# Performance work log

Hardware: AMD Instinct MI355X
Metric: run time of the kernel (lower is better)

## Reference

```python
import math
import jax, jax.numpy as jnp
import numpy as np

N = 4096        # nodes
D = 256         # input_dim
H = 8           # n_heads
HD = D // H     # head_dim
E = 131072      # edges (avg degree 32)
LEAKY_ALPHA = 0.2  # tf.nn.leaky_relu default


def setup_inputs() -> dict:
    key = jax.random.key(0)
    ks = jax.random.split(key, 8)
    inputs = jax.random.normal(ks[0], (N, D), dtype=jnp.float32)
    src = jax.random.randint(ks[1], (E,), 0, N, dtype=jnp.int64)
    dst = jax.random.randint(ks[2], (E,), 0, N, dtype=jnp.int64)
    s = 1.0 / np.sqrt(D).astype(np.float32)
    WQ = jax.random.normal(ks[3], (D, D), dtype=jnp.float32) * s
    WK = jax.random.normal(ks[4], (D, D), dtype=jnp.float32) * s
    WV = jax.random.normal(ks[5], (D, D), dtype=jnp.float32) * s
    Wc = jax.random.normal(ks[6], (D, D), dtype=jnp.float32) * s
    bc = jnp.zeros((D,), dtype=jnp.float32)
    return {"inputs": inputs, "src": src, "dst": dst,
            "WQ": WQ, "WK": WK, "WV": WV, "Wc": Wc, "bc": bc}


def reference(inputs, src, dst, WQ, WK, WV, Wc, bc):
    n, d = inputs.shape
    scale = max(1.0 / math.sqrt(d), 1e-6)
    Q = inputs @ WQ   # [n, d]
    K = inputs @ WK
    V = inputs @ WV
    # Original computes (Q_h K_h^T) @ A with A[src, dst] = 1.
    # Equivalently S[i, j] = Q_h[i] . (sum_{(m, j) in E} K_h[m]) = Q_h @ K2_h^T,
    # where K2 = segment_sum of K rows by edge destination (avoids dense A).
    K2 = jax.ops.segment_sum(K[src], dst, num_segments=n)  # [n, d]
    outs = []
    for h in range(H):  # fixed small head loop, mirrors original per-head loop
        sl = slice(h * HD, (h + 1) * HD)
        S = (Q[:, sl] @ K2[:, sl].T) * scale          # [n, n]
        P = jax.nn.softmax(S, axis=1)
        outs.append(P @ V[:, sl])                     # [n, HD]
    attn = jnp.concatenate(outs, axis=1)              # [n, d]
    h = inputs + attn                                 # residual (no BN at inference)
    h1 = jax.nn.leaky_relu(h @ Wc + bc, negative_slope=LEAKY_ALPHA)
    return h + h1
```

## Files before the change

### kernel.cpp

```cpp
#include <hip/hip_runtime.h>
#include <hip/hip_bf16.h>
#include <math.h>

#define DIM 256
#define HDIM 32
#define NN 4096
#define NM (NN * DIM)
#define PREF 0.09016844005555896f
#define LEAKY 0.2f
#define BCAP 128

typedef __attribute__((ext_vector_type(8))) short short8;
typedef __attribute__((ext_vector_type(16))) float f32x16;

#if __has_builtin(__builtin_amdgcn_exp2f)
#define EXP2(x) __builtin_amdgcn_exp2f(x)
#else
#define EXP2(x) exp2f(x)
#endif

static __device__ __forceinline__ unsigned bfbits(float x) {
  unsigned u = __float_as_uint(x);
  return (u + 0x7fffu + ((u >> 16) & 1u)) >> 16;
}
static __device__ __forceinline__ float bf2f(unsigned short b) {
  return __uint_as_float(((unsigned)b) << 16);
}
static __device__ __forceinline__ unsigned pk_bf16(float lo, float hi) {
  __hip_bfloat162 t = __float22bfloat162_rn(make_float2(lo, hi));
  return *(unsigned*)&t;
}

__global__ __launch_bounds__(256) void convert_w(
    const float* __restrict__ W0, const float* __restrict__ W1,
    const float* __restrict__ W2, const float* __restrict__ W3,
    unsigned short* __restrict__ Wtb, int* __restrict__ cnt) {
  const int tid = threadIdx.x;
  if (blockIdx.y == 0) cnt[blockIdx.x * 256 + tid] = 0;
  __shared__ float tile[64][68];
  const int wsel = blockIdx.y;
  const float* W = wsel == 0 ? W0 : (wsel == 1 ? W1 : (wsel == 2 ? W2 : W3));
  const float scale = wsel == 0 ? PREF : 1.f;
  const int kb = (blockIdx.x & 3) * 64, nb = (blockIdx.x >> 2) * 64;
#pragma unroll
  for (int i = 0; i < 4; ++i) {
    int idx = i * 256 + tid;
    int kr = idx >> 4, ns = idx & 15;
    float4 v = *(const float4*)&W[(kb + kr) * DIM + nb + ns * 4];
    tile[kr][ns * 4 + 0] = v.x; tile[kr][ns * 4 + 1] = v.y;
    tile[kr][ns * 4 + 2] = v.z; tile[kr][ns * 4 + 3] = v.w;
  }
  __syncthreads();
  unsigned short* o = Wtb + wsel * 65536;
#pragma unroll
  for (int i = 0; i < 2; ++i) {
    int idx = i * 256 + tid;
    int nr = idx >> 3, kslot = idx & 7;
    short8 v;
#pragma unroll
    for (int j = 0; j < 8; ++j)
      ((unsigned short*)&v)[j] = (unsigned short)bfbits(tile[kslot * 8 + j][nr] * scale);
    *(short8*)&o[(nb + nr) * DIM + kb + kslot * 8] = v;
  }
}

__global__ __launch_bounds__(256) void gemm_fill(
    const float* __restrict__ inp, const unsigned short* __restrict__ Wtb,
    const int* __restrict__ src, const int* __restrict__ dst, int E,
    int* __restrict__ cnt, int* __restrict__ esrc,
    unsigned short* __restrict__ Qb, unsigned short* __restrict__ Kb,
    unsigned short* __restrict__ Vtb) {
  __shared__ __align__(16) short sA[64 * 256];
  __shared__ __align__(16) short sB[64 * 256];
  const int tid = threadIdx.x;
  const int b = blockIdx.x;
  if (b >= 256) {
    int e = (b - 256) * 256 + tid;
    if (e < E) {
      int d = dst[e];
      int p = atomicAdd(&cnt[d], 1);
      if (p < BCAP) esrc[d * BCAP + p] = src[e];
    }
    return;
  }
  const int m0 = (b & 63) * 64;
  const int n0 = (b >> 6) * 64;
#pragma unroll
  for (int i = 0; i < 16; ++i) {
    int idx = i * 256 + tid;
    int row = idx >> 6, slot = idx & 63;
    float4 v = *(const float4*)&inp[(m0 + row) * DIM + slot * 4];
    uint2 pk = make_uint2(pk_bf16(v.x, v.y), pk_bf16(v.z, v.w));
    int byte = (slot * 8) ^ ((row & 15) << 4);
    *(uint2*)((char*)sA + row * 512 + byte) = pk;
  }
  const int kl = tid & 31, hi = (tid & 63) >> 5, w = tid >> 6;
  const int rw = (w >> 1) * 32, cw = (w & 1) * 32;
  const int arow = rw + kl, brow = cw + kl;
  const int axor = (arow & 15) << 4, bxor = (brow & 15) << 4;
  const char* apA = (const char*)sA + arow * 512;
  const char* apB = (const char*)sB + brow * 512;

#pragma unroll 1
  for (int wsel = 0; wsel < 3; ++wsel) {
    const unsigned short* Wt = Wtb + wsel * 65536;
    __syncthreads();
#pragma unroll
    for (int i = 0; i < 8; ++i) {
      int idx = i * 256 + tid;
      int row = idx >> 5, slot = idx & 31;
      short8 v = *(const short8*)&Wt[(n0 + row) * DIM + slot * 8];
      int byte = (slot * 16) ^ ((row & 15) << 4);
      *(short8*)((char*)sB + row * 512 + byte) = v;
    }
    __syncthreads();
    f32x16 acc;
#pragma unroll
    for (int r = 0; r < 16; ++r) acc[r] = 0.f;
#pragma unroll
    for (int ks = 0; ks < 16; ++ks) {
      int cb = ks * 32 + hi * 16;
      short8 a = *(const short8*)(apA + (cb ^ axor));
      short8 bfr = *(const short8*)(apB + (cb ^ bxor));
      acc = __builtin_amdgcn_mfma_f32_32x32x16_bf16(a, bfr, acc, 0, 0, 0);
    }
    if (wsel < 2) {
      unsigned short* C = wsel == 0 ? Qb : Kb;
#pragma unroll
      for (int r = 0; r < 16; ++r) {
        int mrow = (r & 3) + 8 * (r >> 2) + 4 * hi;
        C[(m0 + rw + mrow) * DIM + n0 + cw + kl] = (unsigned short)bfbits(acc[r]);
      }
    } else {
      __syncthreads();
      unsigned short* tile = (unsigned short*)sB;
#pragma unroll
      for (int r = 0; r < 16; ++r) {
        int mrow = (r & 3) + 8 * (r >> 2) + 4 * hi;
        tile[(rw + mrow) * 72 + cw + kl] = (unsigned short)bfbits(acc[r]);
      }
      __syncthreads();
#pragma unroll
      for (int i = 0; i < 2; ++i) {
        int idx = i * 256 + tid;
        int drow = idx >> 3, nslot = idx & 7;
        short8 v;
#pragma unroll
        for (int j = 0; j < 8; ++j)
          ((unsigned short*)&v)[j] = tile[(nslot * 8 + j) * 72 + drow];
        *(short8*)&Vtb[(n0 + drow) * NN + m0 + nslot * 8] = v;
      }
    }
  }
}

__global__ __launch_bounds__(256) void gather_k2(
    const unsigned short* __restrict__ Kb, const int* __restrict__ cnt,
    const int* __restrict__ esrc, unsigned short* __restrict__ K2b) {
  int w = threadIdx.x >> 6, lane = threadIdx.x & 63;
  int d = blockIdx.x * 4 + w;
  int n = cnt[d]; n = n > BCAP ? BCAP : n;
  const int* eb = esrc + d * BCAP;
  float a0 = 0, a1 = 0, a2 = 0, a3 = 0;
  int j = 0;
  for (; j + 4 <= n; j += 4) {
    int s0 = eb[j], s1 = eb[j + 1], s2 = eb[j + 2], s3 = eb[j + 3];
    ushort4 k0 = *(const ushort4*)&Kb[s0 * DIM + lane * 4];
    ushort4 k1 = *(const ushort4*)&Kb[s1 * DIM + lane * 4];
    ushort4 k2 = *(const ushort4*)&Kb[s2 * DIM + lane * 4];
    ushort4 k3 = *(const ushort4*)&Kb[s3 * DIM + lane * 4];
    a0 += bf2f(k0.x) + bf2f(k1.x) + bf2f(k2.x) + bf2f(k3.x);
    a1 += bf2f(k0.y) + bf2f(k1.y) + bf2f(k2.y) + bf2f(k3.y);
    a2 += bf2f(k0.z) + bf2f(k1.z) + bf2f(k2.z) + bf2f(k3.z);
    a3 += bf2f(k0.w) + bf2f(k1.w) + bf2f(k2.w) + bf2f(k3.w);
  }
  for (; j < n; ++j) {
    int s = eb[j];
    ushort4 kv = *(const ushort4*)&Kb[s * DIM + lane * 4];
    a0 += bf2f(kv.x); a1 += bf2f(kv.y); a2 += bf2f(kv.z); a3 += bf2f(kv.w);
  }
  ushort4 o;
  o.x = bfbits(a0); o.y = bfbits(a1); o.z = bfbits(a2); o.w = bfbits(a3);
  *(ushort4*)&K2b[d * DIM + lane * 4] = o;
}

static __device__ __forceinline__ void compute_tile64(
    const short* __restrict__ lk, const short* __restrict__ lv, int kl, int hi,
    short8 qf0, short8 qf1, f32x16& o, float& lsum) {
#pragma unroll
  for (int sub = 0; sub < 2; ++sub) {
    const int base = sub * 32;
    short8 a0 = *(const short8*)&lk[(base + kl) * 40 + hi * 8];
    short8 a1 = *(const short8*)&lk[(base + kl) * 40 + 16 + hi * 8];
    f32x16 c;
#pragma unroll
    for (int r = 0; r < 16; ++r) c[r] = 0.f;
    __builtin_amdgcn_s_setprio(1);
    c = __builtin_amdgcn_mfma_f32_32x32x16_bf16(a0, qf0, c, 0, 0, 0);
    c = __builtin_amdgcn_mfma_f32_32x32x16_bf16(a1, qf1, c, 0, 0, 0);
    __builtin_amdgcn_s_setprio(0);
    float p[16];
#pragma unroll
    for (int r = 0; r < 16; ++r) p[r] = EXP2(c[r]);
    {
      float t0 = (p[0] + p[1]) + (p[2] + p[3]);
      float t1 = (p[4] + p[5]) + (p[6] + p[7]);
      float t2 = (p[8] + p[9]) + (p[10] + p[11]);
      float t3 = (p[12] + p[13]) + (p[14] + p[15]);
      lsum += (t0 + t1) + (t2 + t3);
    }
    unsigned X0 = pk_bf16(p[0], p[1]);
    unsigned Y0 = pk_bf16(p[2], p[3]);
    unsigned Z0 = pk_bf16(p[4], p[5]);
    unsigned W0 = pk_bf16(p[6], p[7]);
    asm volatile("v_permlane32_swap_b32 %0, %1" : "+v"(X0), "+v"(Z0));
    asm volatile("v_permlane32_swap_b32 %0, %1" : "+v"(Y0), "+v"(W0));
    unsigned X1 = pk_bf16(p[8], p[9]);
    unsigned Y1 = pk_bf16(p[10], p[11]);
    unsigned Z1 = pk_bf16(p[12], p[13]);
    unsigned W1 = pk_bf16(p[14], p[15]);
    asm volatile("v_permlane32_swap_b32 %0, %1" : "+v"(X1), "+v"(Z1));
    asm volatile("v_permlane32_swap_b32 %0, %1" : "+v"(Y1), "+v"(W1));
    short8 pb0, pb1;
    ((unsigned*)&pb0)[0] = X0; ((unsigned*)&pb0)[1] = Y0;
    ((unsigned*)&pb0)[2] = Z0; ((unsigned*)&pb0)[3] = W0;
    ((unsigned*)&pb1)[0] = X1; ((unsigned*)&pb1)[1] = Y1;
    ((unsigned*)&pb1)[2] = Z1; ((unsigned*)&pb1)[3] = W1;
    short8 va0 = *(const short8*)&lv[kl * 72 + base + hi * 8];
    short8 va1 = *(const short8*)&lv[kl * 72 + base + 16 + hi * 8];
    __builtin_amdgcn_s_setprio(1);
    o = __builtin_amdgcn_mfma_f32_32x32x16_bf16(va0, pb0, o, 0, 0, 0);
    o = __builtin_amdgcn_mfma_f32_32x32x16_bf16(va1, pb1, o, 0, 0, 0);
    __builtin_amdgcn_s_setprio(0);
  }
}

__global__ __launch_bounds__(1024, 4) void attn_fused(
    const unsigned short* __restrict__ Qb, const unsigned short* __restrict__ K2b,
    const unsigned short* __restrict__ Vtb, const float* __restrict__ inp,
    unsigned short* __restrict__ Hbf) {
  __shared__ __align__(16) char smem[77824];
  __shared__ float lbuf[8][64];
  const int tid = threadIdx.x;
  const int lane = tid & 63;
  const int wid = tid >> 6;
  const int qw = wid & 1;
  const int zg = wid >> 1;
  const int kl = lane & 31;
  const int hi = lane >> 5;
  const int gtid = tid & 127;
  const int h = blockIdx.y, hc = h * HDIM;
  const int q_local = qw * 32 + kl;
  const int q = blockIdx.x * 64 + q_local;
  const int ks0 = zg * 512;

  short* lk = (short*)smem + zg * 4864;
  short* lv = (short*)smem + zg * 4864 + 2560;

  const int kkey = gtid >> 1, kslot = gtid & 1;
  const int vdim = gtid >> 3, vslot = gtid & 7;
  const unsigned short* kg = &K2b[(ks0 + kkey) * DIM + hc + kslot * 16];
  const unsigned short* vg = &Vtb[(hc + vdim) * NN + ks0 + vslot * 8];
  short* lkw = lk + kkey * 40 + kslot * 16;
  short* lvw = lv + vdim * 72 + vslot * 8;

  short8 qf0 = *(const short8*)&Qb[q * DIM + hc + hi * 8];
  short8 qf1 = *(const short8*)&Qb[q * DIM + hc + 16 + hi * 8];

  f32x16 o;
#pragma unroll
  for (int r = 0; r < 16; ++r) o[r] = 0.f;
  float lsum = 0.f;

#pragma unroll 1
  for (int t = 0; t < 8; ++t) {
    __syncthreads();
    {
      short8 k0 = *(const short8*)(kg);
      short8 k1 = *(const short8*)(kg + 8);
      short8 v0 = *(const short8*)(vg);
      short8 v1 = *(const short8*)(vg + 16 * NN);
      kg += 64 * DIM; vg += 64;
      *(short8*)(lkw) = k0;
      *(short8*)(lkw + 8) = k1;
      *(short8*)(lvw) = v0;
      *(short8*)(lvw + 16 * 72) = v1;
    }
    __syncthreads();
    compute_tile64(lk, lv, kl, hi, qf0, qf1, o, lsum);
  }

  float lt = lsum + __shfl_xor(lsum, 32);
  __syncthreads();
  float* mz = (float*)smem + zg * 2208;
#pragma unroll
  for (int r = 0; r < 16; ++r) {
    int d = (r & 3) + 8 * (r >> 2) + 4 * hi;
    mz[d * 69 + q_local] = o[r];
  }
  if (hi == 0) lbuf[zg][q_local] = lt;
  __syncthreads();
  if (tid < 512) {
    int ql = tid >> 3;
    int dg = (tid & 7) * 4;
    float s = ((lbuf[0][ql] + lbuf[1][ql]) + (lbuf[2][ql] + lbuf[3][ql])) +
              ((lbuf[4][ql] + lbuf[5][ql]) + (lbuf[6][ql] + lbuf[7][ql]));
    float inv = 1.f / s;
    const float* mb = (const float*)smem;
    float acc[4];
#pragma unroll
    for (int i = 0; i < 4; ++i) {
      int off = (dg + i) * 69 + ql;
      acc[i] = ((mb[off] + mb[2208 + off]) + (mb[4416 + off] + mb[6624 + off])) +
               ((mb[8832 + off] + mb[11040 + off]) +
                (mb[13248 + off] + mb[15456 + off]));
    }
    int qg = blockIdx.x * 64 + ql;
    float4 in4 = *(const float4*)&inp[qg * DIM + hc + dg];
    ushort4 hb;
    hb.x = bfbits(in4.x + acc[0] * inv);
    hb.y = bfbits(in4.y + acc[1] * inv);
    hb.z = bfbits(in4.z + acc[2] * inv);
    hb.w = bfbits(in4.w + acc[3] * inv);
    *(ushort4*)&Hbf[qg * DIM + hc + dg] = hb;
  }
}

__global__ __launch_bounds__(256) void gemm_final_mfma(
    const unsigned short* __restrict__ Hbf, const unsigned short* __restrict__ Wct,
    const float* __restrict__ bc, float* __restrict__ out) {
  __shared__ __align__(16) short sA[64 * 256];
  __shared__ __align__(16) short sB[64 * 256];
  const int tid = threadIdx.x;
  const int m0 = blockIdx.x * 64;
  const int n0 = blockIdx.y * 64;
#pragma unroll
  for (int i = 0; i < 8; ++i) {
    int idx = i * 256 + tid;
    int row = idx >> 5, slot = idx & 31;
    short8 v = *(const short8*)&Hbf[(m0 + row) * DIM + slot * 8];
    int byte = (slot * 16) ^ ((row & 15) << 4);
    *(short8*)((char*)sA + row * 512 + byte) = v;
  }
#pragma unroll
  for (int i = 0; i < 8; ++i) {
    int idx = i * 256 + tid;
    int row = idx >> 5, slot = idx & 31;
    short8 v = *(const short8*)&Wct[(n0 + row) * DIM + slot * 8];
    int byte = (slot * 16) ^ ((row & 15) << 4);
    *(short8*)((char*)sB + row * 512 + byte) = v;
  }
  __syncthreads();
  const int kl = tid & 31, hi = (tid & 63) >> 5, w = tid >> 6;
  const int rw = (w >> 1) * 32, cw = (w & 1) * 32;
  const int arow = rw + kl, brow = cw + kl;
  const int axor = (arow & 15) << 4, bxor = (brow & 15) << 4;
  const char* apA = (const char*)sA + arow * 512;
  const char* apB = (const char*)sB + brow * 512;
  f32x16 acc;
#pragma unroll
  for (int r = 0; r < 16; ++r) acc[r] = 0.f;
#pragma unroll
  for (int ks = 0; ks < 16; ++ks) {
    int cb = ks * 32 + hi * 16;
    short8 a = *(const short8*)(apA + (cb ^ axor));
    short8 b = *(const short8*)(apB + (cb ^ bxor));
    acc = __builtin_amdgcn_mfma_f32_32x32x16_bf16(a, b, acc, 0, 0, 0);
  }
#pragma unroll
  for (int r = 0; r < 16; ++r) {
    int mrow = (r & 3) + 8 * (r >> 2) + 4 * hi;
    int lrow = rw + mrow;
    int node = m0 + lrow, col = n0 + cw + kl;
    float x = acc[r] + bc[col];
    x = x > 0.f ? x : LEAKY * x;
    unsigned short hr = *(const unsigned short*)(
        (const char*)sA + lrow * 512 + ((col * 2) ^ ((lrow & 15) << 4)));
    out[node * DIM + col] = bf2f(hr) + x;
  }
}

extern "C" void kernel_launch(void* const* d_in, const int* in_sizes, int n_in,
                              void* d_out, int out_size, void* d_ws, size_t ws_size,
                              hipStream_t stream) {
  const float* inp = (const float*)d_in[0];
  const int* src   = (const int*)d_in[1];
  const int* dst   = (const int*)d_in[2];
  const float* WQ  = (const float*)d_in[3];
  const float* WK  = (const float*)d_in[4];
  const float* WV  = (const float*)d_in[5];
  const float* Wc  = (const float*)d_in[6];
  const float* bc  = (const float*)d_in[7];
  float* out = (float*)d_out;
  const int E = in_sizes[1];

  char* ws = (char*)d_ws;
  unsigned short* Qb  = (unsigned short*)(ws);
  unsigned short* Kb  = (unsigned short*)(ws + 2  * 1024 * 1024);
  unsigned short* Vtb = (unsigned short*)(ws + 4  * 1024 * 1024);
  unsigned short* K2b = (unsigned short*)(ws + 6  * 1024 * 1024);
  unsigned short* Wtb = (unsigned short*)(ws + 8  * 1024 * 1024);
  unsigned short* Hbf = (unsigned short*)(ws + 8 * 1024 * 1024 + 524288);
  int* cnt            = (int*)(ws + 10 * 1024 * 1024 + 524288);
  int* esrc           = (int*)(ws + 10 * 1024 * 1024 + 540672);

  const int fillBlocks = (E + 255) / 256;
  convert_w<<<dim3(16, 4), 256, 0, stream>>>(WQ, WK, WV, Wc, Wtb, cnt);
  gemm_fill<<<256 + fillBlocks, 256, 0, stream>>>(inp, Wtb, src, dst, E, cnt, esrc,
                                                  Qb, Kb, Vtb);
  gather_k2<<<NN / 4, 256, 0, stream>>>(Kb, cnt, esrc, K2b);
  attn_fused<<<dim3(64, 8), 1024, 0, stream>>>(Qb, K2b, Vtb, inp, Hbf);
  gemm_final_mfma<<<dim3(64, 4), 256, 0, stream>>>(Hbf, Wtb + 3 * 65536, bc, out);
}
```

Measured before the change: 88.85 us.

## Load K2/V MFMA operands directly from global, drop LDS staging in attention

The attention kernel now loads each wave's K2 and V MFMA operands straight from global memory into registers, replacing the cooperative LDS tile staging and its per-tile barriers. Blocks shrink from 1024 to 512 threads, each covering 32 queries instead of 64, with twice as many blocks launched. This removes the LDS round trip and the two syncthreads per tile. In exchange, each K2/V row is re-read by more blocks and waves, which leans on the L2 cache, and the global loads may expose latency.

```diff
diff --git a/kernel.cpp b/kernel.cpp
--- a/kernel.cpp
+++ b/kernel.cpp
@@ -184,14 +184,38 @@
   *(ushort4*)&K2b[d * DIM + lane * 4] = o;
 }
 
-static __device__ __forceinline__ void compute_tile64(
-    const short* __restrict__ lk, const short* __restrict__ lv, int kl, int hi,
-    short8 qf0, short8 qf1, f32x16& o, float& lsum) {
-#pragma unroll
-  for (int sub = 0; sub < 2; ++sub) {
-    const int base = sub * 32;
-    short8 a0 = *(const short8*)&lk[(base + kl) * 40 + hi * 8];
-    short8 a1 = *(const short8*)&lk[(base + kl) * 40 + 16 + hi * 8];
+__global__ __launch_bounds__(512, 4) void attn_fused(
+    const unsigned short* __restrict__ Qb, const unsigned short* __restrict__ K2b,
+    const unsigned short* __restrict__ Vtb, const float* __restrict__ inp,
+    unsigned short* __restrict__ Hbf) {
+  __shared__ float mz[8][32 * 33];
+  __shared__ float lbuf[8][32];
+  const int tid = threadIdx.x;
+  const int lane = tid & 63;
+  const int zg = tid >> 6;
+  const int kl = lane & 31;
+  const int hi = lane >> 5;
+  const int h = blockIdx.y, hc = h * HDIM;
+  const int q = blockIdx.x * 32 + kl;
+
+  short8 qf0 = *(const short8*)&Qb[q * DIM + hc + hi * 8];
+  short8 qf1 = *(const short8*)&Qb[q * DIM + hc + 16 + hi * 8];
+
+  const unsigned short* kp = &K2b[(zg * 512 + kl) * DIM + hc + hi * 8];
+  const unsigned short* vp = &Vtb[(hc + kl) * NN + zg * 512 + hi * 8];
+
+  f32x16 o;
+#pragma unroll
+  for (int r = 0; r < 16; ++r) o[r] = 0.f;
+  float lsum = 0.f;
+
+#pragma unroll 2
+  for (int sub = 0; sub < 16; ++sub) {
+    short8 a0 = *(const short8*)(kp);
+    short8 a1 = *(const short8*)(kp + 16);
+    short8 va0 = *(const short8*)(vp);
+    short8 va1 = *(const short8*)(vp + 16);
+    kp += 32 * DIM; vp += 32;
     f32x16 c;
 #pragma unroll
     for (int r = 0; r < 16; ++r) c[r] = 0.f;
@@ -226,96 +250,35 @@
     ((unsigned*)&pb0)[2] = Z0; ((unsigned*)&pb0)[3] = W0;
     ((unsigned*)&pb1)[0] = X1; ((unsigned*)&pb1)[1] = Y1;
     ((unsigned*)&pb1)[2] = Z1; ((unsigned*)&pb1)[3] = W1;
-    short8 va0 = *(const short8*)&lv[kl * 72 + base + hi * 8];
-    short8 va1 = *(const short8*)&lv[kl * 72 + base + 16 + hi * 8];
     __builtin_amdgcn_s_setprio(1);
     o = __builtin_amdgcn_mfma_f32_32x32x16_bf16(va0, pb0, o, 0, 0, 0);
     o = __builtin_amdgcn_mfma_f32_32x32x16_bf16(va1, pb1, o, 0, 0, 0);
     __builtin_amdgcn_s_setprio(0);
   }
-}
-
-__global__ __launch_bounds__(1024, 4) void attn_fused(
-    const unsigned short* __restrict__ Qb, const unsigned short* __restrict__ K2b,
-    const unsigned short* __restrict__ Vtb, const float* __restrict__ inp,
-    unsigned short* __restrict__ Hbf) {
-  __shared__ __align__(16) char smem[77824];
-  __shared__ float lbuf[8][64];
-  const int tid = threadIdx.x;
-  const int lane = tid & 63;
-  const int wid = tid >> 6;
-  const int qw = wid & 1;
-  const int zg = wid >> 1;
-  const int kl = lane & 31;
-  const int hi = lane >> 5;
-  const int gtid = tid & 127;
-  const int h = blockIdx.y, hc = h * HDIM;
-  const int q_local = qw * 32 + kl;
-  const int q = blockIdx.x * 64 + q_local;
-  const int ks0 = zg * 512;
-
-  short* lk = (short*)smem + zg * 4864;
-  short* lv = (short*)smem + zg * 4864 + 2560;
-
-  const int kkey = gtid >> 1, kslot = gtid & 1;
-  const int vdim = gtid >> 3, vslot = gtid & 7;
-  const unsigned short* kg = &K2b[(ks0 + kkey) * DIM + hc + kslot * 16];
-  const unsigned short* vg = &Vtb[(hc + vdim) * NN + ks0 + vslot * 8];
-  short* lkw = lk + kkey * 40 + kslot * 16;
-  short* lvw = lv + vdim * 72 + vslot * 8;
-
-  short8 qf0 = *(const short8*)&Qb[q * DIM + hc + hi * 8];
-  short8 qf1 = *(const short8*)&Qb[q * DIM + hc + 16 + hi * 8];
-
-  f32x16 o;
-#pragma unroll
-  for (int r = 0; r < 16; ++r) o[r] = 0.f;
-  float lsum = 0.f;
-
-#pragma unroll 1
-  for (int t = 0; t < 8; ++t) {
-    __syncthreads();
-    {
-      short8 k0 = *(const short8*)(kg);
-      short8 k1 = *(const short8*)(kg + 8);
-      short8 v0 = *(const short8*)(vg);
-      short8 v1 = *(const short8*)(vg + 16 * NN);
-      kg += 64 * DIM; vg += 64;
-      *(short8*)(lkw) = k0;
-      *(short8*)(lkw + 8) = k1;
-      *(short8*)(lvw) = v0;
-      *(short8*)(lvw + 16 * 72) = v1;
-    }
-    __syncthreads();
-    compute_tile64(lk, lv, kl, hi, qf0, qf1, o, lsum);
-  }
 
   float lt = lsum + __shfl_xor(lsum, 32);
-  __syncthreads();
-  float* mz = (float*)smem + zg * 2208;
+  float* m = mz[zg];
 #pragma unroll
   for (int r = 0; r < 16; ++r) {
     int d = (r & 3) + 8 * (r >> 2) + 4 * hi;
-    mz[d * 69 + q_local] = o[r];
-  }
-  if (hi == 0) lbuf[zg][q_local] = lt;
+    m[d * 33 + kl] = o[r];
+  }
+  if (hi == 0) lbuf[zg][kl] = lt;
   __syncthreads();
-  if (tid < 512) {
+  if (tid < 256) {
     int ql = tid >> 3;
     int dg = (tid & 7) * 4;
     float s = ((lbuf[0][ql] + lbuf[1][ql]) + (lbuf[2][ql] + lbuf[3][ql])) +
               ((lbuf[4][ql] + lbuf[5][ql]) + (lbuf[6][ql] + lbuf[7][ql]));
     float inv = 1.f / s;
-    const float* mb = (const float*)smem;
     float acc[4];
 #pragma unroll
     for (int i = 0; i < 4; ++i) {
-      int off = (dg + i) * 69 + ql;
-      acc[i] = ((mb[off] + mb[2208 + off]) + (mb[4416 + off] + mb[6624 + off])) +
-               ((mb[8832 + off] + mb[11040 + off]) +
-                (mb[13248 + off] + mb[15456 + off]));
-    }
-    int qg = blockIdx.x * 64 + ql;
+      int off = (dg + i) * 33 + ql;
+      acc[i] = ((mz[0][off] + mz[1][off]) + (mz[2][off] + mz[3][off])) +
+               ((mz[4][off] + mz[5][off]) + (mz[6][off] + mz[7][off]));
+    }
+    int qg = blockIdx.x * 32 + ql;
     float4 in4 = *(const float4*)&inp[qg * DIM + hc + dg];
     ushort4 hb;
     hb.x = bfbits(in4.x + acc[0] * inv);
@@ -409,6 +372,6 @@
   gemm_fill<<<256 + fillBlocks, 256, 0, stream>>>(inp, Wtb, src, dst, E, cnt, esrc,
                                                   Qb, Kb, Vtb);
   gather_k2<<<NN / 4, 256, 0, stream>>>(Kb, cnt, esrc, K2b);
-  attn_fused<<<dim3(64, 8), 1024, 0, stream>>>(Qb, K2b, Vtb, inp, Hbf);
+  attn_fused<<<dim3(128, 8), 512, 0, stream>>>(Qb, K2b, Vtb, inp, Hbf);
   gemm_final_mfma<<<dim3(64, 4), 256, 0, stream>>>(Hbf, Wtb + 3 * 65536, bc, out);
 }
```

Result: slower. 101.1 us (+13.8%).
